# Optimization experiments

Measured on AMD Instinct MI355X. Metric: run time of the kernel, lower is better.

## Reference

```python
import jax, jax.numpy as jnp
import numpy as np

CH = 512
COND = 1280
HEADS = 8
GROUPS = CH // 8
EPS = 1e-5


def conv2d(x, w, b, pad):
    y = jax.lax.conv_general_dilated(
        x, w, window_strides=(1, 1), padding=[(pad, pad), (pad, pad)],
        dimension_numbers=('NCHW', 'OIHW', 'NCHW'))
    return y + b[None, :, None, None]


def group_norm(x, gamma, beta, groups, eps=EPS):
    b, c, h, w = x.shape
    xg = x.reshape(b, groups, c // groups, h, w)
    mu = xg.mean(axis=(2, 3, 4), keepdims=True)
    var = xg.var(axis=(2, 3, 4), keepdims=True)
    xn = ((xg - mu) * jax.lax.rsqrt(var + eps)).reshape(b, c, h, w)
    return xn * gamma[None, :, None, None] + beta[None, :, None, None]


def setup_inputs() -> dict:
    key = jax.random.key(0)
    ks = jax.random.split(key, 20)
    s = 0.05
    inp = {
        'x': jax.random.normal(ks[0], (8, CH, 32, 32), jnp.float32),
        'conditioning': jax.random.normal(ks[1], (8, COND), jnp.float32),
        # ResBlock params
        'c1w': jax.random.normal(ks[2], (CH, CH, 3, 3), jnp.float32) * s,
        'c1b': jnp.zeros((CH,), jnp.float32),
        'g1w': jnp.ones((CH,), jnp.float32),
        'g1b': jnp.zeros((CH,), jnp.float32),
        'c2w': jax.random.normal(ks[3], (CH, CH, 3, 3), jnp.float32) * s,
        'c2b': jnp.zeros((CH,), jnp.float32),
        'g2w': jnp.ones((CH,), jnp.float32),
        'g2b': jnp.zeros((CH,), jnp.float32),
        'cpw': jax.random.normal(ks[4], (CH, COND), jnp.float32) * s,
        'cpb': jnp.zeros((CH,), jnp.float32),
        'rpw': jax.random.normal(ks[5], (CH, CH, 1, 1), jnp.float32) * s,
        'rpb': jnp.zeros((CH,), jnp.float32),
        # Attention params (1x1 convs)
        'qw': jax.random.normal(ks[6], (CH, CH, 1, 1), jnp.float32) * s,
        'qb': jnp.zeros((CH,), jnp.float32),
        'kw': jax.random.normal(ks[7], (CH, CH, 1, 1), jnp.float32) * s,
        'kb': jnp.zeros((CH,), jnp.float32),
        'vw': jax.random.normal(ks[8], (CH, CH, 1, 1), jnp.float32) * s,
        'vb': jnp.zeros((CH,), jnp.float32),
        'ow': jax.random.normal(ks[9], (CH, CH, 1, 1), jnp.float32) * s,
        'ob': jnp.zeros((CH,), jnp.float32),
    }
    return inp


def reference(x, conditioning, c1w, c1b, g1w, g1b, c2w, c2b, g2w, g2b,
              cpw, cpb, rpw, rpb, qw, qb, kw, kb, vw, vb, ow, ob):
    # --- ResBlock ---
    residual = conv2d(x, rpw, rpb, 0)
    h = conv2d(x, c1w, c1b, 1)
    h = group_norm(h, g1w, g1b, GROUPS)
    h = jax.nn.silu(h)
    h = conv2d(h, c2w, c2b, 1)
    h = group_norm(h, g2w, g2b, GROUPS)
    cond = conditioning @ cpw.T + cpb  # [B, C]
    h = h * (1.0 + cond[:, :, None, None]) + residual

    # --- SpatialSelfAttention ---
    b, c, hh, ww = h.shape
    d = c // HEADS
    scale = d ** (-0.5)
    q = conv2d(h, qw, qb, 0).reshape(b, HEADS, d, hh * ww)
    k = conv2d(h, kw, kb, 0).reshape(b, HEADS, d, hh * ww)
    v = conv2d(h, vw, vb, 0).reshape(b, HEADS, d, hh * ww)
    attn = jnp.einsum('bhdn,bhdm->bhnm', q, k) * scale  # [B,H,N,N]
    attn = jax.nn.softmax(attn, axis=-1)
    out = jnp.einsum('bhnm,bhdm->bhdn', attn, v).reshape(b, c, hh, ww)
    return conv2d(out, ow, ob, 0) + h
```

## Files before the change

kernel.cpp:

```cpp
#include <hip/hip_runtime.h>
#include <hip/hip_bf16.h>

typedef unsigned short u16;
typedef __attribute__((ext_vector_type(8))) short bf8;
typedef __attribute__((ext_vector_type(4))) short bf4;
typedef __attribute__((ext_vector_type(4))) float f32x4;

#define CH_ 512
#define NSP 1024
#define NB 8
#define CONDDIM 1280
#define NGROUP 64
#define HEADS_ 8
#define HD 64
#define PR 34
#define PPB (PR*PR)

#define VWAIT(N) asm volatile("s_waitcnt vmcnt(" #N ")" ::: "memory")
#define SCHEDB __builtin_amdgcn_sched_barrier(0)
#define BARRIER do { SCHEDB; __builtin_amdgcn_s_barrier(); SCHEDB; } while (0)

__device__ __forceinline__ u16 f2bf(float f) {
  union { float f; unsigned u; } v; v.f = f;
  unsigned u = v.u;
  return (u16)((u + 0x7fffu + ((u >> 16) & 1u)) >> 16);
}

__device__ __forceinline__ unsigned cvt_pk_bf16(float lo, float hi) {
  unsigned r;
  asm volatile("v_cvt_pk_bf16_f32 %0, %1, %2" : "=v"(r) : "v"(lo), "v"(hi));
  return r;
}

__device__ __forceinline__ f32x4 mfma_bf16(bf8 a, bf8 b, f32x4 c) {
  return __builtin_amdgcn_mfma_f32_16x16x32_bf16(a, b, c, 0, 0, 0);
}

__device__ __forceinline__ void gload16(const void* g, void* l) {
  __builtin_amdgcn_global_load_lds((const __attribute__((address_space(1))) void*)g,
                                   (__attribute__((address_space(3))) void*)l, 16, 0, 0);
}


__global__ __launch_bounds__(1024) void pack_x_kernel(const float* __restrict__ x, u16* __restrict__ xp) {
  __shared__ float t[32][33];
  int b = blockIdx.z;
  int c0 = blockIdx.y * 32, p0 = blockIdx.x * 32;
  int tx = threadIdx.x & 31, ty = threadIdx.x >> 5;
  t[ty][tx] = x[((size_t)b * CH_ + c0 + ty) * NSP + p0 + tx];
  __syncthreads();
  int p = p0 + ty;
  int y = p >> 5, xc = p & 31;
  xp[((size_t)b * PPB + (size_t)(y + 1) * PR + xc + 1) * CH_ + c0 + tx] = f2bf(t[tx][ty]);
}

__global__ __launch_bounds__(256) void border_zero_kernel(u16* __restrict__ a, u16* __restrict__ b) {
  int id = blockIdx.x * 256 + threadIdx.x;
  if (id >= NB * 132 * 64) return;
  int ch8 = id & 63;
  int rest = id >> 6;
  int bidx = rest % 132;
  int bb = rest / 132;
  int r, c;
  if (bidx < 34)       { r = 0;          c = bidx; }
  else if (bidx < 68)  { r = 33;         c = bidx - 34; }
  else if (bidx < 100) { r = bidx - 67;  c = 0; }
  else                 { r = bidx - 99;  c = 33; }
  size_t off = ((size_t)bb * PPB + (size_t)r * PR + c) * CH_ + ch8 * 8;
  const bf8 z = {0, 0, 0, 0, 0, 0, 0, 0};
  *(bf8*)(a + off) = z;
  *(bf8*)(b + off) = z;
}

__global__ __launch_bounds__(256) void pack_w3_kernel(const float* __restrict__ w, u16* __restrict__ wp) {
  int id = blockIdx.x * 256 + threadIdx.x;
  if (id >= 9 * 64 * CH_) return;
  int co = id & (CH_ - 1);
  int cib = (id >> 9) & 63;
  int t = id >> 15;
  int dy = t / 3, dx = t % 3;
  bf8 v;
#pragma unroll
  for (int j = 0; j < 8; j++) {
    int ci = cib * 8 + j;
    v[j] = (short)f2bf(w[(((size_t)co * CH_ + ci) * 3 + dy) * 3 + dx]);
  }
  *(bf8*)(wp + ((size_t)(t * 64 + cib) * CH_ + co) * 8) = v;
}

__global__ __launch_bounds__(256) void pack_w1_kernel(const float* __restrict__ w, u16* __restrict__ wp) {
  int id = blockIdx.x * 256 + threadIdx.x;
  if (id >= 64 * CH_) return;
  int co = id & (CH_ - 1);
  int cib = id >> 9;
  bf8 v;
#pragma unroll
  for (int j = 0; j < 8; j++) v[j] = (short)f2bf(w[(size_t)co * CH_ + cib * 8 + j]);
  *(bf8*)(wp + ((size_t)cib * CH_ + co) * 8) = v;
}

__global__ __launch_bounds__(256) void cond_kernel(const float* __restrict__ cd, const float* __restrict__ cpw,
                                                   const float* __restrict__ cpb, float* __restrict__ cond) {
  int b = blockIdx.y;
  int c = blockIdx.x * 4 + (threadIdx.x >> 6);
  int lane = threadIdx.x & 63;
  const float* wrow = cpw + (size_t)c * CONDDIM;
  const float* crow = cd + (size_t)b * CONDDIM;
  float s = 0.f;
  for (int i = lane; i < CONDDIM; i += 64) s += crow[i] * wrow[i];
#pragma unroll
  for (int m = 32; m > 0; m >>= 1) s += __shfl_xor(s, m, 64);
  if (lane == 0) cond[b * CH_ + c] = s + cpb[c];
}

template <int TAPS, int PIN, int EPI>
__global__ __launch_bounds__(256, TAPS == 9 ? 4 : 3) void conv_kernel(
    const u16* __restrict__ in, const u16* __restrict__ wp, const float* __restrict__ bias,
    float* __restrict__ outf, const float* __restrict__ addf,
    u16* __restrict__ o0, u16* __restrict__ o1, u16* __restrict__ o2,
    const float* __restrict__ b0, const float* __restrict__ b1, const float* __restrict__ b2) {
  constexpr int LDSZ = (TAPS == 9) ? (2 * 14336 + 3 * 4096) : (4 * 8192 + 4 * 4096);
  __shared__ char lds[LDSZ];
  char* ldsA = lds;
  char* ldsB = lds + ((TAPS == 9) ? 2 * 14336 : 4 * 8192);

  const int b = blockIdx.z;
  int seg = 0, coy = blockIdx.y;
  if constexpr (EPI == 5) { seg = coy >> 3; coy &= 7; }
  const int co0 = coy * 64;
  const int p0 = blockIdx.x * 128;
  const int tid = threadIdx.x;
  const int lane = tid & 63, wid = tid >> 6;
  const int wv = wid >> 1, wc = wid & 1;
  const int l15 = lane & 15, lhi = lane >> 4;

  const char* aSrc;
  if constexpr (TAPS == 9) {
    aSrc = (const char*)in + ((size_t)b * PPB + (size_t)blockIdx.x * 4 * PR) * 1024;
  } else if constexpr (PIN) {
    aSrc = (const char*)in + (size_t)b * PPB * 1024;
  } else {
    aSrc = (const char*)in + ((size_t)b * NSP + p0) * 1024;
  }
  const char* bSrc = (const char*)wp + (size_t)((EPI == 5) ? seg * 524288 : 0) + co0 * 16;

  const int pB = ((tid >> 6) * 512 + (tid & 63)) * 16;
  int pA0, pA1, pA3 = 0;
  if constexpr (TAPS == 9) {
    pA0 = ((tid >> 2) << 10) + ((tid & 3) << 4);
    pA3 = ((192 + ((tid & 127) >> 2)) << 10) + ((tid & 3) << 4);
    pA1 = 0;
  } else {
    int a0 = (tid >> 2), a1 = 64 + (tid >> 2);
    if constexpr (PIN) {
      int pp0 = p0 + a0, pp1 = p0 + a1;
      int g0 = ((pp0 >> 5) + 1) * PR + (pp0 & 31) + 1;
      int g1 = ((pp1 >> 5) + 1) * PR + (pp1 & 31) + 1;
      pA0 = (g0 << 10) + ((tid & 3) << 4);
      pA1 = (g1 << 10) + ((tid & 3) << 4);
    } else {
      pA0 = (a0 << 10) + ((tid & 3) << 4);
      pA1 = (a1 << 10) + ((tid & 3) << 4);
    }
  }

  const int aAddr = (TAPS == 9) ? ((wv * 68 + l15) * 64 + lhi * 16)
                                : ((wv * 64 + l15) * 64 + lhi * 16);
  const int bAddr = (lhi * 64 + wc * 32 + l15) * 16;

  f32x4 acc[4][2];
#pragma unroll
  for (int m = 0; m < 4; m++)
#pragma unroll
    for (int n = 0; n < 2; n++) acc[m][n] = {0.f, 0.f, 0.f, 0.f};

  if constexpr (TAPS == 9) {
    gload16(aSrc + pA0,          ldsA + (wid << 10));
    gload16(aSrc + pA0 + 65536,  ldsA + 4096 + (wid << 10));
    gload16(aSrc + pA0 + 131072, ldsA + 8192 + (wid << 10));
    gload16(aSrc + pA3,          ldsA + 12288 + ((wid & 1) << 10));
    gload16(bSrc + pB,           ldsB + (wid << 10));
    gload16(bSrc + 524288 + pB,  ldsB + 4096 + (wid << 10));
    VWAIT(1);
    BARRIER;

#define PH9(KC, T, AS) do {                                                             \
    constexpr int DT = ((T) / 3) * 34 + ((T) % 3);                                      \
    const int kcn_ = ((KC) < 15) ? (KC) + 1 : 15;                                       \
    { const int kb_ = ((T) >= 7) ? kcn_ : (KC);                                         \
      constexpr int TB = ((T) + 2) % 9;                                                 \
      gload16(bSrc + (size_t)(TB * 64 + kb_ * 4) * 8192 + pB,                           \
              ldsB + (((T) + 2) % 3) * 4096 + (wid << 10)); }                           \
    if constexpr ((T) >= 4 && (T) < 7)                                                  \
      gload16(aSrc + kcn_ * 64 + pA0 + ((T) - 4) * 65536,                               \
              ldsA + (1 - (AS)) * 14336 + ((T) - 4) * 4096 + (wid << 10));              \
    if constexpr ((T) == 7)                                                             \
      gload16(aSrc + kcn_ * 64 + pA3,                                                   \
              ldsA + (1 - (AS)) * 14336 + 12288 + ((wid & 1) << 10));                   \
    SCHEDB;                                                                             \
    bf8 af0 = *(const bf8*)(ldsA + (AS) * 14336 + DT * 64 + 0    + aAddr);              \
    bf8 af1 = *(const bf8*)(ldsA + (AS) * 14336 + DT * 64 + 1024 + aAddr);              \
    bf8 af2 = *(const bf8*)(ldsA + (AS) * 14336 + DT * 64 + 2176 + aAddr);              \
    bf8 af3 = *(const bf8*)(ldsA + (AS) * 14336 + DT * 64 + 3200 + aAddr);              \
    bf8 bq0 = *(const bf8*)(ldsB + ((T) % 3) * 4096 + 0   + bAddr);                     \
    bf8 bq1 = *(const bf8*)(ldsB + ((T) % 3) * 4096 + 256 + bAddr);                     \
    __builtin_amdgcn_s_setprio(1);                                                      \
    acc[0][0] = mfma_bf16(af0, bq0, acc[0][0]);                                         \
    acc[0][1] = mfma_bf16(af0, bq1, acc[0][1]);                                         \
    acc[1][0] = mfma_bf16(af1, bq0, acc[1][0]);                                         \
    acc[1][1] = mfma_bf16(af1, bq1, acc[1][1]);                                         \
    acc[2][0] = mfma_bf16(af2, bq0, acc[2][0]);                                         \
    acc[2][1] = mfma_bf16(af2, bq1, acc[2][1]);                                         \
    acc[3][0] = mfma_bf16(af3, bq0, acc[3][0]);                                         \
    acc[3][1] = mfma_bf16(af3, bq1, acc[3][1]);                                         \
    __builtin_amdgcn_s_setprio(0);                                                      \
    if constexpr ((T) >= 4 && (T) <= 7) { VWAIT(2); } else { VWAIT(1); }                \
    BARRIER;                                                                            \
  } while (0)

    for (int kc2 = 0; kc2 < 8; kc2++) {
      PH9(kc2 * 2, 0, 0); PH9(kc2 * 2, 1, 0); PH9(kc2 * 2, 2, 0);
      PH9(kc2 * 2, 3, 0); PH9(kc2 * 2, 4, 0); PH9(kc2 * 2, 5, 0);
      PH9(kc2 * 2, 6, 0); PH9(kc2 * 2, 7, 0); PH9(kc2 * 2, 8, 0);
      PH9(kc2 * 2 + 1, 0, 1); PH9(kc2 * 2 + 1, 1, 1); PH9(kc2 * 2 + 1, 2, 1);
      PH9(kc2 * 2 + 1, 3, 1); PH9(kc2 * 2 + 1, 4, 1); PH9(kc2 * 2 + 1, 5, 1);
      PH9(kc2 * 2 + 1, 6, 1); PH9(kc2 * 2 + 1, 7, 1); PH9(kc2 * 2 + 1, 8, 1);
    }
#undef PH9
  } else {
    gload16(aSrc + pA0,         ldsA + (wid << 10));
    gload16(aSrc + pA1,         ldsA + 4096 + (wid << 10));
    gload16(bSrc + pB,          ldsB + (wid << 10));
    gload16(aSrc + 64 + pA0,    ldsA + 8192 + (wid << 10));
    gload16(aSrc + 64 + pA1,    ldsA + 8192 + 4096 + (wid << 10));
    gload16(bSrc + 32768 + pB,  ldsB + 4096 + (wid << 10));
    VWAIT(3);
    BARRIER;

#define PH1(KC, S) do {                                                                 \
    constexpr int S2 = ((S) + 2) & 3;                                                   \
    const int kcn_ = ((KC) + 2 < 16) ? (KC) + 2 : 15;                                   \
    gload16(bSrc + (size_t)kcn_ * 32768 + pB, ldsB + S2 * 4096 + (wid << 10));          \
    gload16(aSrc + kcn_ * 64 + pA0, ldsA + S2 * 8192 + (wid << 10));                    \
    gload16(aSrc + kcn_ * 64 + pA1, ldsA + S2 * 8192 + 4096 + (wid << 10));             \
    SCHEDB;                                                                             \
    bf8 af0 = *(const bf8*)(ldsA + (S) * 8192 + 0    + aAddr);                          \
    bf8 af1 = *(const bf8*)(ldsA + (S) * 8192 + 1024 + aAddr);                          \
    bf8 af2 = *(const bf8*)(ldsA + (S) * 8192 + 2048 + aAddr);                          \
    bf8 af3 = *(const bf8*)(ldsA + (S) * 8192 + 3072 + aAddr);                          \
    bf8 bq0 = *(const bf8*)(ldsB + (S) * 4096 + 0   + bAddr);                           \
    bf8 bq1 = *(const bf8*)(ldsB + (S) * 4096 + 256 + bAddr);                           \
    __builtin_amdgcn_s_setprio(1);                                                      \
    acc[0][0] = mfma_bf16(af0, bq0, acc[0][0]);                                         \
    acc[0][1] = mfma_bf16(af0, bq1, acc[0][1]);                                         \
    acc[1][0] = mfma_bf16(af1, bq0, acc[1][0]);                                         \
    acc[1][1] = mfma_bf16(af1, bq1, acc[1][1]);                                         \
    acc[2][0] = mfma_bf16(af2, bq0, acc[2][0]);                                         \
    acc[2][1] = mfma_bf16(af2, bq1, acc[2][1]);                                         \
    acc[3][0] = mfma_bf16(af3, bq0, acc[3][0]);                                         \
    acc[3][1] = mfma_bf16(af3, bq1, acc[3][1]);                                         \
    __builtin_amdgcn_s_setprio(0);                                                      \
    VWAIT(3);                                                                           \
    BARRIER;                                                                            \
  } while (0)

    for (int kc4 = 0; kc4 < 4; kc4++) {
      PH1(kc4 * 4 + 0, 0); PH1(kc4 * 4 + 1, 1); PH1(kc4 * 4 + 2, 2); PH1(kc4 * 4 + 3, 3);
    }
#undef PH1
  }

  VWAIT(0);

#pragma unroll
  for (int m = 0; m < 4; m++) {
    int pbase = p0 + wv * 64 + m * 16 + lhi * 4;
#pragma unroll
    for (int n = 0; n < 2; n++) {
      int co = co0 + wc * 32 + n * 16 + l15;
      if constexpr (EPI == 0) {
        float bv = bias[co];
#pragma unroll
        for (int r = 0; r < 4; r++)
          outf[((size_t)b * NSP + pbase + r) * CH_ + co] = acc[m][n][r] + bv;
      } else if constexpr (EPI == 2) {
        float bv = bias[co];
        f32x4 v;
#pragma unroll
        for (int r = 0; r < 4; r++)
          v[r] = acc[m][n][r] + bv + addf[((size_t)b * NSP + pbase + r) * CH_ + co];
        *(f32x4*)(outf + ((size_t)b * CH_ + co) * NSP + pbase) = v;
      } else {
        if (seg == 0) {
          float bv = b0[co];
#pragma unroll
          for (int r = 0; r < 4; r++)
            o0[((size_t)b * NSP + pbase + r) * CH_ + co] = f2bf((acc[m][n][r] + bv) * 0.125f);
        } else if (seg == 1) {
          float bv = b1[co];
#pragma unroll
          for (int r = 0; r < 4; r++)
            o1[((size_t)b * NSP + pbase + r) * CH_ + co] = f2bf(acc[m][n][r] + bv);
        } else {
          float bv = b2[co];
          union { bf4 v; unsigned long long u; } pk4;
#pragma unroll
          for (int r = 0; r < 4; r++) pk4.v[r] = (short)f2bf(acc[m][n][r] + bv);
          *(unsigned long long*)(o2 + ((size_t)b * CH_ + co) * NSP + pbase) = pk4.u;
        }
      }
    }
  }
}

template <int MODE>
__global__ __launch_bounds__(256) void gn_kernel(
    const float* __restrict__ in, const float* __restrict__ gw, const float* __restrict__ gb,
    const float* __restrict__ cond, const float* __restrict__ resid,
    float* __restrict__ outf, u16* __restrict__ outb) {
  int b = blockIdx.y, g = blockIdx.x;
  int tid = threadIdx.x;
  int c = g * 8 + (tid & 7);
  int prow = tid >> 3;
  const float* base = in + (size_t)b * NSP * CH_ + c;
  float v[32];
  float s = 0.f, ss = 0.f;
#pragma unroll
  for (int i = 0; i < 32; i++) {
    v[i] = base[(size_t)(prow + i * 32) * CH_];
    s += v[i]; ss += v[i] * v[i];
  }
  __shared__ float rs[256], rss[256];
  rs[tid] = s; rss[tid] = ss;
  __syncthreads();
  for (int off = 128; off > 0; off >>= 1) {
    if (tid < off) { rs[tid] += rs[tid + off]; rss[tid] += rss[tid + off]; }
    __syncthreads();
  }
  float mean = rs[0] * (1.f / 8192.f);
  float var = rss[0] * (1.f / 8192.f) - mean * mean;
  float inv = rsqrtf(var + 1e-5f);
  float gamma = gw[c], beta = gb[c];
  float cm = 0.f;
  if (MODE == 1) cm = 1.f + cond[b * CH_ + c];
#pragma unroll
  for (int i = 0; i < 32; i++) {
    int p = prow + i * 32;
    float y = (v[i] - mean) * inv * gamma + beta;
    if (MODE == 0) {
      float sg = 1.f / (1.f + __expf(-y));
      int yy = p >> 5, xc = p & 31;
      outb[((size_t)b * PPB + (size_t)(yy + 1) * PR + xc + 1) * CH_ + c] = f2bf(y * sg);
    } else {
      size_t idx = ((size_t)b * NSP + p) * CH_ + c;
      float z = y * cm + resid[idx];
      outf[idx] = z;
      outb[idx] = f2bf(z);
    }
  }
}

__global__ __launch_bounds__(256) void attn_kernel(const u16* __restrict__ q, const u16* __restrict__ k,
                                                   const u16* __restrict__ vT, u16* __restrict__ ao) {
  int bid = blockIdx.x;
  int swz = (bid & 7) * 64 + (bid >> 3);
  int b = swz >> 6;
  int head = (swz >> 3) & 7;
  int qt = swz & 7;
  int tid = threadIdx.x, lane = tid & 63, wid = tid >> 6;
  int l15 = lane & 15, lhi = lane >> 4;
  int cb = head * HD;
  int q0 = qt * 128 + wid * 32;

  const char* qp = (const char*)(q + (size_t)b * NSP * CH_ + cb);
  const char* kp = (const char*)(k + (size_t)b * NSP * CH_ + cb);
  const char* vp = (const char*)(vT + ((size_t)b * CH_ + cb) * NSP);

  __shared__ u16 Ksh[2][64 * 64];
  __shared__ u16 Vsh[2][64 * 64];

  bf8 aq[2][2];
#pragma unroll
  for (int qh = 0; qh < 2; qh++)
#pragma unroll
    for (int ks = 0; ks < 2; ks++)
      aq[qh][ks] = *(const bf8*)(qp + ((size_t)(q0 + qh * 16 + l15) * CH_ + ks * 32 + lhi * 8) * 2);

  f32x4 o[2][4];
  float mrow[2], lrow[2];
#pragma unroll
  for (int qh = 0; qh < 2; qh++) {
    mrow[qh] = -1e30f; lrow[qh] = 0.f;
#pragma unroll
    for (int n = 0; n < 4; n++) o[qh][n] = {0.f, 0.f, 0.f, 0.f};
  }

  auto stage = [&](int kt, int buf) {
#pragma unroll
    for (int t = 0; t < 2; t++) {
      int i = wid * 2 + t;
      int chunk = i * 64 + lane;
      int r = chunk >> 3, c = chunk & 7;
      gload16(kp + (size_t)(kt * 64 + r) * 1024 + (size_t)((c ^ (r & 7)) * 16),
              (char*)Ksh[buf] + i * 1024);
    }
#pragma unroll
    for (int t = 0; t < 2; t++) {
      int i = wid * 2 + t;
      int chunk = i * 64 + lane;
      int r = chunk >> 3, c = chunk & 7;
      gload16(vp + (size_t)r * 2048 + (size_t)(kt * 128) + (size_t)((c ^ (r & 7)) * 16),
              (char*)Vsh[buf] + i * 1024);
    }
  };

  stage(0, 0);

  for (int kt = 0; kt < 16; ++kt) {
    __syncthreads();
    if (kt < 15) stage(kt + 1, (kt + 1) & 1);
    const char* Kb = (const char*)Ksh[kt & 1];
    const char* Vb = (const char*)Vsh[kt & 1];

    f32x4 sacc[2][4];
#pragma unroll
    for (int qh = 0; qh < 2; qh++)
#pragma unroll
      for (int kf = 0; kf < 4; kf++) sacc[qh][kf] = {0.f, 0.f, 0.f, 0.f};

#pragma unroll
    for (int kf = 0; kf < 4; kf++) {
      bf8 ak[2];
#pragma unroll
      for (int ks = 0; ks < 2; ks++)
        ak[ks] = *(const bf8*)(Kb + (size_t)(kf * 16 + l15) * 128 + (((ks * 4 + lhi) ^ (l15 & 7)) * 16));
#pragma unroll
      for (int qh = 0; qh < 2; qh++)
#pragma unroll
        for (int ks = 0; ks < 2; ks++)
          sacc[qh][kf] = mfma_bf16(ak[ks], aq[qh][ks], sacc[qh][kf]);
    }

    unsigned pk[2][4][2];
#pragma unroll
    for (int qh = 0; qh < 2; qh++) {
      float pmax = sacc[qh][0][0];
#pragma unroll
      for (int kf = 0; kf < 4; kf++)
#pragma unroll
        for (int r = 0; r < 4; r++) pmax = fmaxf(pmax, sacc[qh][kf][r]);
      pmax = fmaxf(pmax, __shfl_xor(pmax, 16, 64));
      pmax = fmaxf(pmax, __shfl_xor(pmax, 32, 64));
      float mn = fmaxf(mrow[qh], pmax);
      float corr = __expf(mrow[qh] - mn);
      mrow[qh] = mn;
      float rsum = 0.f;
#pragma unroll
      for (int kf = 0; kf < 4; kf++) {
        f32x4 pv;
#pragma unroll
        for (int r = 0; r < 4; r++) {
          pv[r] = __expf(sacc[qh][kf][r] - mn);
          rsum += pv[r];
        }
        pk[qh][kf][0] = cvt_pk_bf16(pv[0], pv[1]);
        pk[qh][kf][1] = cvt_pk_bf16(pv[2], pv[3]);
      }
      rsum += __shfl_xor(rsum, 16, 64);
      rsum += __shfl_xor(rsum, 32, 64);
      lrow[qh] = lrow[qh] * corr + rsum;
      float corr_o[4];
#pragma unroll
      for (int r = 0; r < 4; r++) corr_o[r] = __shfl(corr, lhi * 4 + r, 64);
#pragma unroll
      for (int n = 0; n < 4; n++)
#pragma unroll
        for (int r = 0; r < 4; r++) o[qh][n][r] *= corr_o[r];
    }

#pragma unroll
    for (int g = 0; g < 2; g++) {
      union { bf8 v8; unsigned u[4]; } ap[2];
#pragma unroll
      for (int qh = 0; qh < 2; qh++) {
        ap[qh].u[0] = pk[qh][2 * g][0];
        ap[qh].u[1] = pk[qh][2 * g][1];
        ap[qh].u[2] = pk[qh][2 * g + 1][0];
        ap[qh].u[3] = pk[qh][2 * g + 1][1];
      }
#pragma unroll
      for (int nf2 = 0; nf2 < 4; nf2++) {
        int row = nf2 * 16 + l15;
        int c0 = 4 * g + (lhi >> 1);
        union { bf8 v8; bf4 v4[2]; } bv;
        bv.v4[0] = *(const bf4*)(Vb + (size_t)row * 128 + ((c0 ^ (l15 & 7)) * 16) + (lhi & 1) * 8);
        bv.v4[1] = *(const bf4*)(Vb + (size_t)row * 128 + (((c0 + 2) ^ (l15 & 7)) * 16) + (lhi & 1) * 8);
#pragma unroll
        for (int qh = 0; qh < 2; qh++)
          o[qh][nf2] = mfma_bf16(ap[qh].v8, bv.v8, o[qh][nf2]);
      }
    }
  }

#pragma unroll
  for (int qh = 0; qh < 2; qh++) {
    float linv[4];
#pragma unroll
    for (int r = 0; r < 4; r++) linv[r] = 1.f / __shfl(lrow[qh], lhi * 4 + r, 64);
#pragma unroll
    for (int nf2 = 0; nf2 < 4; nf2++)
#pragma unroll
      for (int r = 0; r < 4; r++) {
        float val = o[qh][nf2][r] * linv[r];
        ao[((size_t)b * NSP + q0 + qh * 16 + lhi * 4 + r) * CH_ + cb + nf2 * 16 + l15] = f2bf(val);
      }
  }
}


extern "C" void kernel_launch(void* const* d_in, const int* in_sizes, int n_in,
                              void* d_out, int out_size, void* d_ws, size_t ws_size,
                              hipStream_t stream) {
  const float* x    = (const float*)d_in[0];
  const float* cnd  = (const float*)d_in[1];
  const float* c1w  = (const float*)d_in[2];
  const float* c1b  = (const float*)d_in[3];
  const float* g1w  = (const float*)d_in[4];
  const float* g1b  = (const float*)d_in[5];
  const float* c2w  = (const float*)d_in[6];
  const float* c2b  = (const float*)d_in[7];
  const float* g2w  = (const float*)d_in[8];
  const float* g2b  = (const float*)d_in[9];
  const float* cpw  = (const float*)d_in[10];
  const float* cpb  = (const float*)d_in[11];
  const float* rpw  = (const float*)d_in[12];
  const float* rpb  = (const float*)d_in[13];
  const float* qw   = (const float*)d_in[14];
  const float* qb   = (const float*)d_in[15];
  const float* kw   = (const float*)d_in[16];
  const float* kb   = (const float*)d_in[17];
  const float* vw   = (const float*)d_in[18];
  const float* vb   = (const float*)d_in[19];
  const float* ow   = (const float*)d_in[20];
  const float* ob   = (const float*)d_in[21];
  float* out = (float*)d_out;

  char* ws = (char*)d_ws;
  size_t off = 0;
  auto alloc = [&](size_t bytes) -> char* {
    char* p = ws + off;
    off = (off + bytes + 255) & ~(size_t)255;
    return p;
  };
  const size_t ACT_F = (size_t)NB * NSP * CH_ * 4;
  const size_t ACT_B = (size_t)NB * NSP * CH_ * 2;
  const size_t PAD_B = (size_t)NB * PPB * CH_ * 2;

  u16* xp    = (u16*)alloc(PAD_B);
  u16* h1p   = (u16*)alloc(PAD_B);
  u16* w1p   = (u16*)alloc((size_t)9 * CH_ * CH_ * 2);
  u16* w2p   = (u16*)alloc((size_t)9 * CH_ * CH_ * 2);
  u16* wrp   = (u16*)alloc((size_t)CH_ * CH_ * 2);
  u16* wqkv  = (u16*)alloc((size_t)3 * CH_ * CH_ * 2);
  u16* wop   = (u16*)alloc((size_t)CH_ * CH_ * 2);
  float* cndv = (float*)alloc((size_t)NB * CH_ * 4);
  float* resid = (float*)alloc(ACT_F);
  float* h12  = (float*)alloc(ACT_F);
  u16* hb    = (u16*)alloc(ACT_B);
  u16* qbuf  = (u16*)alloc(ACT_B);
  u16* kbuf  = (u16*)alloc(ACT_B);
  u16* vTb   = (u16*)alloc(ACT_B);
  u16* aob   = (u16*)alloc(ACT_B);
  if (off > ws_size) return;

  dim3 tgrid(NSP / 32, CH_ / 32, NB);
  border_zero_kernel<<<(NB * 132 * 64 + 255) / 256, 256, 0, stream>>>(xp, h1p);
  pack_x_kernel<<<tgrid, 1024, 0, stream>>>(x, xp);
  pack_w3_kernel<<<(9 * 64 * CH_ + 255) / 256, 256, 0, stream>>>(c1w, w1p);
  pack_w3_kernel<<<(9 * 64 * CH_ + 255) / 256, 256, 0, stream>>>(c2w, w2p);
  pack_w1_kernel<<<(64 * CH_) / 256, 256, 0, stream>>>(rpw, wrp);
  pack_w1_kernel<<<(64 * CH_) / 256, 256, 0, stream>>>(qw, wqkv);
  pack_w1_kernel<<<(64 * CH_) / 256, 256, 0, stream>>>(kw, wqkv + (size_t)CH_ * CH_);
  pack_w1_kernel<<<(64 * CH_) / 256, 256, 0, stream>>>(vw, wqkv + (size_t)2 * CH_ * CH_);
  pack_w1_kernel<<<(64 * CH_) / 256, 256, 0, stream>>>(ow, wop);
  cond_kernel<<<dim3(CH_ / 4, NB), 256, 0, stream>>>(cnd, cpw, cpb, cndv);

  dim3 ggrid(NSP / 128, CH_ / 64, NB);
  dim3 qgrid(NSP / 128, 3 * CH_ / 64, NB);
  conv_kernel<9, 1, 0><<<ggrid, 256, 0, stream>>>(xp, w1p, c1b, h12, nullptr,
                                                  nullptr, nullptr, nullptr, nullptr, nullptr, nullptr);
  conv_kernel<1, 1, 0><<<ggrid, 256, 0, stream>>>(xp, wrp, rpb, resid, nullptr,
                                                  nullptr, nullptr, nullptr, nullptr, nullptr, nullptr);
  gn_kernel<0><<<dim3(NGROUP, NB), 256, 0, stream>>>(h12, g1w, g1b, nullptr, nullptr, nullptr, h1p);
  conv_kernel<9, 1, 0><<<ggrid, 256, 0, stream>>>(h1p, w2p, c2b, h12, nullptr,
                                                  nullptr, nullptr, nullptr, nullptr, nullptr, nullptr);
  gn_kernel<1><<<dim3(NGROUP, NB), 256, 0, stream>>>(h12, g2w, g2b, cndv, resid, h12, hb);
  conv_kernel<1, 0, 5><<<qgrid, 256, 0, stream>>>(hb, wqkv, nullptr, nullptr, nullptr,
                                                  qbuf, kbuf, vTb, qb, kb, vb);
  attn_kernel<<<512, 256, 0, stream>>>(qbuf, kbuf, vTb, aob);
  conv_kernel<1, 0, 2><<<ggrid, 256, 0, stream>>>(aob, wop, ob, out, h12,
                                                  nullptr, nullptr, nullptr, nullptr, nullptr, nullptr);
}
```

Measured before the change: 259.3 us.

## Halve attention query tile, fold log2e into Q scale, add lazy softmax rescale

The attention kernel now gives each wave 16 query rows instead of 32 and launches 1024 blocks instead of 512, with launch bounds raised to 4 blocks per CU for more occupancy. The softmax scale now includes log2(e), so the kernel can use exp2f directly. The running-max rescale of the output accumulator is skipped unless the new block max exceeds the old one by more than 8 in log2 units. The smaller query tile means each K/V tile loaded into shared memory serves fewer queries, which doubles K/V traffic. The lazy rescale also lets unnormalized exponentials grow up to 2^8 before correction.

```diff
diff --git a/kernel.cpp b/kernel.cpp
--- a/kernel.cpp
+++ b/kernel.cpp
@@ -15,6 +15,7 @@
 #define HD 64
 #define PR 34
 #define PPB (PR*PR)
+#define QSCALE 0.18033688011112042f
 
 #define VWAIT(N) asm volatile("s_waitcnt vmcnt(" #N ")" ::: "memory")
 #define SCHEDB __builtin_amdgcn_sched_barrier(0)
@@ -295,7 +296,7 @@
           float bv = b0[co];
 #pragma unroll
           for (int r = 0; r < 4; r++)
-            o0[((size_t)b * NSP + pbase + r) * CH_ + co] = f2bf((acc[m][n][r] + bv) * 0.125f);
+            o0[((size_t)b * NSP + pbase + r) * CH_ + co] = f2bf((acc[m][n][r] + bv) * QSCALE);
         } else if (seg == 1) {
           float bv = b1[co];
 #pragma unroll
@@ -360,17 +361,17 @@
   }
 }
 
-__global__ __launch_bounds__(256) void attn_kernel(const u16* __restrict__ q, const u16* __restrict__ k,
-                                                   const u16* __restrict__ vT, u16* __restrict__ ao) {
+__global__ __launch_bounds__(256, 4) void attn_kernel(const u16* __restrict__ q, const u16* __restrict__ k,
+                                                      const u16* __restrict__ vT, u16* __restrict__ ao) {
   int bid = blockIdx.x;
-  int swz = (bid & 7) * 64 + (bid >> 3);
-  int b = swz >> 6;
-  int head = (swz >> 3) & 7;
-  int qt = swz & 7;
+  int swz = (bid & 7) * 128 + (bid >> 3);
+  int b = swz >> 7;
+  int head = (swz >> 4) & 7;
+  int qt = swz & 15;
   int tid = threadIdx.x, lane = tid & 63, wid = tid >> 6;
   int l15 = lane & 15, lhi = lane >> 4;
   int cb = head * HD;
-  int q0 = qt * 128 + wid * 32;
+  int q0 = qt * 64 + wid * 16;
 
   const char* qp = (const char*)(q + (size_t)b * NSP * CH_ + cb);
   const char* kp = (const char*)(k + (size_t)b * NSP * CH_ + cb);
@@ -379,21 +380,15 @@
   __shared__ u16 Ksh[2][64 * 64];
   __shared__ u16 Vsh[2][64 * 64];
 
-  bf8 aq[2][2];
-#pragma unroll
-  for (int qh = 0; qh < 2; qh++)
-#pragma unroll
-    for (int ks = 0; ks < 2; ks++)
-      aq[qh][ks] = *(const bf8*)(qp + ((size_t)(q0 + qh * 16 + l15) * CH_ + ks * 32 + lhi * 8) * 2);
-
-  f32x4 o[2][4];
-  float mrow[2], lrow[2];
-#pragma unroll
-  for (int qh = 0; qh < 2; qh++) {
-    mrow[qh] = -1e30f; lrow[qh] = 0.f;
-#pragma unroll
-    for (int n = 0; n < 4; n++) o[qh][n] = {0.f, 0.f, 0.f, 0.f};
-  }
+  bf8 aq[2];
+#pragma unroll
+  for (int ks = 0; ks < 2; ks++)
+    aq[ks] = *(const bf8*)(qp + ((size_t)(q0 + l15) * CH_ + ks * 32 + lhi * 8) * 2);
+
+  f32x4 o[4];
+#pragma unroll
+  for (int n = 0; n < 4; n++) o[n] = {0.f, 0.f, 0.f, 0.f};
+  float mrow = -1e30f, lrow = 0.f;
 
   auto stage = [&](int kt, int buf) {
 #pragma unroll
@@ -422,12 +417,9 @@
     const char* Kb = (const char*)Ksh[kt & 1];
     const char* Vb = (const char*)Vsh[kt & 1];
 
-    f32x4 sacc[2][4];
-#pragma unroll
-    for (int qh = 0; qh < 2; qh++)
-#pragma unroll
-      for (int kf = 0; kf < 4; kf++) sacc[qh][kf] = {0.f, 0.f, 0.f, 0.f};
-
+    f32x4 sacc[4];
+#pragma unroll
+    for (int kf = 0; kf < 4; kf++) sacc[kf] = {0.f, 0.f, 0.f, 0.f};
 #pragma unroll
     for (int kf = 0; kf < 4; kf++) {
       bf8 ak[2];
@@ -435,59 +427,57 @@
       for (int ks = 0; ks < 2; ks++)
         ak[ks] = *(const bf8*)(Kb + (size_t)(kf * 16 + l15) * 128 + (((ks * 4 + lhi) ^ (l15 & 7)) * 16));
 #pragma unroll
-      for (int qh = 0; qh < 2; qh++)
-#pragma unroll
-        for (int ks = 0; ks < 2; ks++)
-          sacc[qh][kf] = mfma_bf16(ak[ks], aq[qh][ks], sacc[qh][kf]);
-    }
-
-    unsigned pk[2][4][2];
-#pragma unroll
-    for (int qh = 0; qh < 2; qh++) {
-      float pmax = sacc[qh][0][0];
-#pragma unroll
-      for (int kf = 0; kf < 4; kf++)
-#pragma unroll
-        for (int r = 0; r < 4; r++) pmax = fmaxf(pmax, sacc[qh][kf][r]);
-      pmax = fmaxf(pmax, __shfl_xor(pmax, 16, 64));
-      pmax = fmaxf(pmax, __shfl_xor(pmax, 32, 64));
-      float mn = fmaxf(mrow[qh], pmax);
-      float corr = __expf(mrow[qh] - mn);
-      mrow[qh] = mn;
-      float rsum = 0.f;
-#pragma unroll
-      for (int kf = 0; kf < 4; kf++) {
-        f32x4 pv;
-#pragma unroll
-        for (int r = 0; r < 4; r++) {
-          pv[r] = __expf(sacc[qh][kf][r] - mn);
-          rsum += pv[r];
-        }
-        pk[qh][kf][0] = cvt_pk_bf16(pv[0], pv[1]);
-        pk[qh][kf][1] = cvt_pk_bf16(pv[2], pv[3]);
+      for (int ks = 0; ks < 2; ks++)
+        sacc[kf] = mfma_bf16(ak[ks], aq[ks], sacc[kf]);
+    }
+
+    float pmax;
+    {
+      float m0 = fmaxf(fmaxf(sacc[0][0], sacc[0][1]), fmaxf(sacc[0][2], sacc[0][3]));
+      float m1 = fmaxf(fmaxf(sacc[1][0], sacc[1][1]), fmaxf(sacc[1][2], sacc[1][3]));
+      float m2 = fmaxf(fmaxf(sacc[2][0], sacc[2][1]), fmaxf(sacc[2][2], sacc[2][3]));
+      float m3 = fmaxf(fmaxf(sacc[3][0], sacc[3][1]), fmaxf(sacc[3][2], sacc[3][3]));
+      pmax = fmaxf(fmaxf(m0, m1), fmaxf(m2, m3));
+    }
+    pmax = fmaxf(pmax, __shfl_xor(pmax, 16, 64));
+    pmax = fmaxf(pmax, __shfl_xor(pmax, 32, 64));
+    if (__any(pmax > mrow + 8.f)) {
+      float mn = fmaxf(mrow, pmax);
+      float corr = exp2f(mrow - mn);
+      mrow = mn;
+      lrow *= corr;
+      float corr_o[4];
+#pragma unroll
+      for (int r = 0; r < 4; r++) corr_o[r] = __shfl(corr, lhi * 4 + r, 64);
+#pragma unroll
+      for (int n = 0; n < 4; n++)
+#pragma unroll
+        for (int r = 0; r < 4; r++) o[n][r] *= corr_o[r];
+    }
+    unsigned pk[4][2];
+    float rsum = 0.f;
+#pragma unroll
+    for (int kf = 0; kf < 4; kf++) {
+      f32x4 pv;
+#pragma unroll
+      for (int r = 0; r < 4; r++) {
+        pv[r] = exp2f(sacc[kf][r] - mrow);
+        rsum += pv[r];
       }
-      rsum += __shfl_xor(rsum, 16, 64);
-      rsum += __shfl_xor(rsum, 32, 64);
-      lrow[qh] = lrow[qh] * corr + rsum;
-      float corr_o[4];
-#pragma unroll
-      for (int r = 0; r < 4; r++) corr_o[r] = __shfl(corr, lhi * 4 + r, 64);
-#pragma unroll
-      for (int n = 0; n < 4; n++)
-#pragma unroll
-        for (int r = 0; r < 4; r++) o[qh][n][r] *= corr_o[r];
-    }
+      pk[kf][0] = cvt_pk_bf16(pv[0], pv[1]);
+      pk[kf][1] = cvt_pk_bf16(pv[2], pv[3]);
+    }
+    rsum += __shfl_xor(rsum, 16, 64);
+    rsum += __shfl_xor(rsum, 32, 64);
+    lrow += rsum;
 
 #pragma unroll
     for (int g = 0; g < 2; g++) {
-      union { bf8 v8; unsigned u[4]; } ap[2];
-#pragma unroll
-      for (int qh = 0; qh < 2; qh++) {
-        ap[qh].u[0] = pk[qh][2 * g][0];
-        ap[qh].u[1] = pk[qh][2 * g][1];
-        ap[qh].u[2] = pk[qh][2 * g + 1][0];
-        ap[qh].u[3] = pk[qh][2 * g + 1][1];
-      }
+      union { bf8 v8; unsigned u[4]; } ap;
+      ap.u[0] = pk[2 * g][0];
+      ap.u[1] = pk[2 * g][1];
+      ap.u[2] = pk[2 * g + 1][0];
+      ap.u[3] = pk[2 * g + 1][1];
 #pragma unroll
       for (int nf2 = 0; nf2 < 4; nf2++) {
         int row = nf2 * 16 + l15;
@@ -495,26 +485,21 @@
         union { bf8 v8; bf4 v4[2]; } bv;
         bv.v4[0] = *(const bf4*)(Vb + (size_t)row * 128 + ((c0 ^ (l15 & 7)) * 16) + (lhi & 1) * 8);
         bv.v4[1] = *(const bf4*)(Vb + (size_t)row * 128 + (((c0 + 2) ^ (l15 & 7)) * 16) + (lhi & 1) * 8);
-#pragma unroll
-        for (int qh = 0; qh < 2; qh++)
-          o[qh][nf2] = mfma_bf16(ap[qh].v8, bv.v8, o[qh][nf2]);
+        o[nf2] = mfma_bf16(ap.v8, bv.v8, o[nf2]);
       }
     }
   }
 
-#pragma unroll
-  for (int qh = 0; qh < 2; qh++) {
-    float linv[4];
-#pragma unroll
-    for (int r = 0; r < 4; r++) linv[r] = 1.f / __shfl(lrow[qh], lhi * 4 + r, 64);
-#pragma unroll
-    for (int nf2 = 0; nf2 < 4; nf2++)
-#pragma unroll
-      for (int r = 0; r < 4; r++) {
-        float val = o[qh][nf2][r] * linv[r];
-        ao[((size_t)b * NSP + q0 + qh * 16 + lhi * 4 + r) * CH_ + cb + nf2 * 16 + l15] = f2bf(val);
-      }
-  }
+  float linv[4];
+#pragma unroll
+  for (int r = 0; r < 4; r++) linv[r] = 1.f / __shfl(lrow, lhi * 4 + r, 64);
+#pragma unroll
+  for (int nf2 = 0; nf2 < 4; nf2++)
+#pragma unroll
+    for (int r = 0; r < 4; r++) {
+      float val = o[nf2][r] * linv[r];
+      ao[((size_t)b * NSP + q0 + lhi * 4 + r) * CH_ + cb + nf2 * 16 + l15] = f2bf(val);
+    }
 }
 
 
@@ -597,7 +582,7 @@
   gn_kernel<1><<<dim3(NGROUP, NB), 256, 0, stream>>>(h12, g2w, g2b, cndv, resid, h12, hb);
   conv_kernel<1, 0, 5><<<qgrid, 256, 0, stream>>>(hb, wqkv, nullptr, nullptr, nullptr,
                                                   qbuf, kbuf, vTb, qb, kb, vb);
-  attn_kernel<<<512, 256, 0, stream>>>(qbuf, kbuf, vTb, aob);
+  attn_kernel<<<1024, 256, 0, stream>>>(qbuf, kbuf, vTb, aob);
   conv_kernel<1, 0, 2><<<ggrid, 256, 0, stream>>>(aob, wop, ob, out, h12,
                                                   nullptr, nullptr, nullptr, nullptr, nullptr, nullptr);
 }
```

Result: no change. 263.8 us (+1.8%).

## Triple-buffer attention K/V loads and use lazy exp2 softmax rescaling

Applied to the files above, without the earlier changes.

The attention kernel moves from double to triple buffering of K/V tiles in LDS, prefetching two tiles ahead and using explicit vmcnt waits with one barrier per iteration instead of __syncthreads. Softmax now works in base 2: log2(e) is folded into the Q scale in the projection epilogue and exp2f replaces __expf. The running max and output rescale are only updated when some row's tile max exceeds the stored max by more than 8, and row-sum cross-lane reductions are deferred to the end. This cuts shuffles and rescale work per tile but uses more LDS, which may reduce occupancy, and allows unnormalized exponentials up to 2^8.

```diff
diff --git a/kernel.cpp b/kernel.cpp
--- a/kernel.cpp
+++ b/kernel.cpp
@@ -15,6 +15,7 @@
 #define HD 64
 #define PR 34
 #define PPB (PR*PR)
+#define QSCALE 0.18033688011112042f
 
 #define VWAIT(N) asm volatile("s_waitcnt vmcnt(" #N ")" ::: "memory")
 #define SCHEDB __builtin_amdgcn_sched_barrier(0)
@@ -295,7 +296,7 @@
           float bv = b0[co];
 #pragma unroll
           for (int r = 0; r < 4; r++)
-            o0[((size_t)b * NSP + pbase + r) * CH_ + co] = f2bf((acc[m][n][r] + bv) * 0.125f);
+            o0[((size_t)b * NSP + pbase + r) * CH_ + co] = f2bf((acc[m][n][r] + bv) * QSCALE);
         } else if (seg == 1) {
           float bv = b1[co];
 #pragma unroll
@@ -376,8 +377,8 @@
   const char* kp = (const char*)(k + (size_t)b * NSP * CH_ + cb);
   const char* vp = (const char*)(vT + ((size_t)b * CH_ + cb) * NSP);
 
-  __shared__ u16 Ksh[2][64 * 64];
-  __shared__ u16 Vsh[2][64 * 64];
+  __shared__ u16 Ksh[3][64 * 64];
+  __shared__ u16 Vsh[3][64 * 64];
 
   bf8 aq[2][2];
 #pragma unroll
@@ -387,10 +388,10 @@
       aq[qh][ks] = *(const bf8*)(qp + ((size_t)(q0 + qh * 16 + l15) * CH_ + ks * 32 + lhi * 8) * 2);
 
   f32x4 o[2][4];
-  float mrow[2], lrow[2];
+  float mrow[2], lpart[2];
 #pragma unroll
   for (int qh = 0; qh < 2; qh++) {
-    mrow[qh] = -1e30f; lrow[qh] = 0.f;
+    mrow[qh] = -1e30f; lpart[qh] = 0.f;
 #pragma unroll
     for (int n = 0; n < 4; n++) o[qh][n] = {0.f, 0.f, 0.f, 0.f};
   }
@@ -415,12 +416,15 @@
   };
 
   stage(0, 0);
-
+  stage(1, 1);
+
+  int cB = 0, sB = 2;
   for (int kt = 0; kt < 16; ++kt) {
-    __syncthreads();
-    if (kt < 15) stage(kt + 1, (kt + 1) & 1);
-    const char* Kb = (const char*)Ksh[kt & 1];
-    const char* Vb = (const char*)Vsh[kt & 1];
+    if (kt < 15) { VWAIT(4); } else { VWAIT(0); }
+    BARRIER;
+    if (kt < 14) stage(kt + 2, sB);
+    const char* Kb = (const char*)Ksh[0] + cB * 8192;
+    const char* Vb = (const char*)Vsh[0] + cB * 8192;
 
     f32x4 sacc[2][4];
 #pragma unroll
@@ -444,38 +448,39 @@
     unsigned pk[2][4][2];
 #pragma unroll
     for (int qh = 0; qh < 2; qh++) {
-      float pmax = sacc[qh][0][0];
-#pragma unroll
-      for (int kf = 0; kf < 4; kf++)
-#pragma unroll
-        for (int r = 0; r < 4; r++) pmax = fmaxf(pmax, sacc[qh][kf][r]);
-      pmax = fmaxf(pmax, __shfl_xor(pmax, 16, 64));
-      pmax = fmaxf(pmax, __shfl_xor(pmax, 32, 64));
-      float mn = fmaxf(mrow[qh], pmax);
-      float corr = __expf(mrow[qh] - mn);
-      mrow[qh] = mn;
+      float m0 = fmaxf(fmaxf(sacc[qh][0][0], sacc[qh][0][1]), fmaxf(sacc[qh][0][2], sacc[qh][0][3]));
+      float m1 = fmaxf(fmaxf(sacc[qh][1][0], sacc[qh][1][1]), fmaxf(sacc[qh][1][2], sacc[qh][1][3]));
+      float m2 = fmaxf(fmaxf(sacc[qh][2][0], sacc[qh][2][1]), fmaxf(sacc[qh][2][2], sacc[qh][2][3]));
+      float m3 = fmaxf(fmaxf(sacc[qh][3][0], sacc[qh][3][1]), fmaxf(sacc[qh][3][2], sacc[qh][3][3]));
+      float pml = fmaxf(fmaxf(m0, m1), fmaxf(m2, m3));
+      if (__any(pml > mrow[qh] + 8.f)) {
+        float pm = fmaxf(pml, __shfl_xor(pml, 16, 64));
+        pm = fmaxf(pm, __shfl_xor(pm, 32, 64));
+        float mn = fmaxf(mrow[qh], pm);
+        float corr = exp2f(mrow[qh] - mn);
+        mrow[qh] = mn;
+        lpart[qh] *= corr;
+        float corr_o[4];
+#pragma unroll
+        for (int r = 0; r < 4; r++) corr_o[r] = __shfl(corr, lhi * 4 + r, 64);
+#pragma unroll
+        for (int n = 0; n < 4; n++)
+#pragma unroll
+          for (int r = 0; r < 4; r++) o[qh][n][r] *= corr_o[r];
+      }
       float rsum = 0.f;
 #pragma unroll
       for (int kf = 0; kf < 4; kf++) {
         f32x4 pv;
 #pragma unroll
         for (int r = 0; r < 4; r++) {
-          pv[r] = __expf(sacc[qh][kf][r] - mn);
+          pv[r] = exp2f(sacc[qh][kf][r] - mrow[qh]);
           rsum += pv[r];
         }
         pk[qh][kf][0] = cvt_pk_bf16(pv[0], pv[1]);
         pk[qh][kf][1] = cvt_pk_bf16(pv[2], pv[3]);
       }
-      rsum += __shfl_xor(rsum, 16, 64);
-      rsum += __shfl_xor(rsum, 32, 64);
-      lrow[qh] = lrow[qh] * corr + rsum;
-      float corr_o[4];
-#pragma unroll
-      for (int r = 0; r < 4; r++) corr_o[r] = __shfl(corr, lhi * 4 + r, 64);
-#pragma unroll
-      for (int n = 0; n < 4; n++)
-#pragma unroll
-        for (int r = 0; r < 4; r++) o[qh][n][r] *= corr_o[r];
+      lpart[qh] += rsum;
     }
 
 #pragma unroll
@@ -500,13 +505,19 @@
           o[qh][nf2] = mfma_bf16(ap[qh].v8, bv.v8, o[qh][nf2]);
       }
     }
+
+    cB = (cB == 2) ? 0 : cB + 1;
+    sB = (sB == 2) ? 0 : sB + 1;
   }
 
 #pragma unroll
   for (int qh = 0; qh < 2; qh++) {
+    float lrow = lpart[qh];
+    lrow += __shfl_xor(lrow, 16, 64);
+    lrow += __shfl_xor(lrow, 32, 64);
     float linv[4];
 #pragma unroll
-    for (int r = 0; r < 4; r++) linv[r] = 1.f / __shfl(lrow[qh], lhi * 4 + r, 64);
+    for (int r = 0; r < 4; r++) linv[r] = 1.f / __shfl(lrow, lhi * 4 + r, 64);
 #pragma unroll
     for (int nf2 = 0; nf2 < 4; nf2++)
 #pragma unroll
```

Result: slower. 265.2 us (+2.3%).
